# Kernel tuning notes

Measured on AMD Instinct MI355X. Metric: run time of the kernel, lower is better.

The kernel has to match this reference:

```python
import jax, jax.numpy as jnp
import numpy as np
import math

D = 512
LAMBDA_DRIFT = 0.3

def _sinusoid(pos, d):
    # pos: [B, T] float positions (1..T); returns [B, T, d]
    half = d // 2
    div = jnp.exp(-math.log(10000.0) * (2.0 * jnp.arange(half, dtype=jnp.float32) / d))
    ang = pos[..., None] * div  # [B,T,half]
    pe = jnp.stack([jnp.sin(ang), jnp.cos(ang)], axis=-1)  # [B,T,half,2]
    return pe.reshape(pos.shape + (d,))

def _lin(x, W, b):
    return x @ W + b

def setup_inputs() -> dict:
    key = jax.random.key(0)
    ks = jax.random.split(key, 30)
    B, T, L = 4, 16, 1024
    def w(k, fan_in, fan_out):
        return jax.random.normal(k, (fan_in, fan_out), dtype=jnp.float32) / np.sqrt(fan_in)
    inp = {
        'x': jax.random.normal(ks[0], (B, L, D), dtype=jnp.float32),
        'memory_snapshot': jax.random.normal(ks[1], (B, T, L, D), dtype=jnp.float32),
        'delta_W': w(ks[2], D, D), 'delta_b': jnp.zeros((D,), jnp.float32),
        'xproj_W': w(ks[3], D, D), 'xproj_b': jnp.zeros((D,), jnp.float32),
        'phys_W': w(ks[4], D, D), 'phys_b': jnp.zeros((D,), jnp.float32),
        'gate_W': w(ks[5], 3 * D, D), 'gate_b': jnp.zeros((D,), jnp.float32),
        'outp_W': w(ks[6], D, D), 'outp_b': jnp.zeros((D,), jnp.float32),
        'seq_W': w(ks[7], D, D), 'seq_b': jnp.zeros((D,), jnp.float32),
        'q_W': w(ks[8], D, D), 'q_b': jnp.zeros((D,), jnp.float32),
        'mem_W': w(ks[9], D, D), 'mem_b': jnp.zeros((D,), jnp.float32),
        'curd_W': w(ks[10], D, D), 'curd_b': jnp.zeros((D,), jnp.float32),
        'memd_W': w(ks[11], D, D), 'memd_b': jnp.zeros((D,), jnp.float32),
        'fuse_W': w(ks[12], 2 * D, D), 'fuse_b': jnp.zeros((D,), jnp.float32),
    }
    return inp

def reference(x, memory_snapshot,
              delta_W, delta_b, xproj_W, xproj_b, phys_W, phys_b,
              gate_W, gate_b, outp_W, outp_b, seq_W, seq_b,
              q_W, q_b, mem_W, mem_b, curd_W, curd_b,
              memd_W, memd_b, fuse_W, fuse_b):
    B, T, L, Dm = memory_snapshot.shape
    # physical trajectory = last memory slot
    x_phys = memory_snapshot[:, -1]                      # [B,L,D]
    # --- DriftCorrectionExtractor ---
    delta = x - x_phys
    delta_feat = _lin(delta, delta_W, delta_b)
    x_feat = _lin(x, xproj_W, xproj_b)
    phys_feat = _lin(x_phys, phys_W, phys_b)
    g = jax.nn.sigmoid(_lin(jnp.concatenate([delta, x, x_phys], -1), gate_W, gate_b))
    raw_memory = _lin(g * delta_feat + (1.0 - g) * (x_feat - phys_feat), outp_W, outp_b)
    # --- sequential positional embedding on memory time axis ---
    pos = jnp.broadcast_to(jnp.arange(1, T + 1, dtype=jnp.float32)[None, :], (B, T))
    pos_emb = _lin(_sinusoid(pos, Dm), seq_W, seq_b)     # [B,T,D]
    memory = memory_snapshot + pos_emb[:, :, None, :]    # [B,T,L,D]
    # --- content score ---
    q_global = _lin((x + raw_memory).mean(axis=1), q_W, q_b)        # [B,D]
    memory_global = _lin(memory.mean(axis=2), mem_W, mem_b)          # [B,T,D]
    content_score = jnp.einsum('bd,btd->bt', q_global, memory_global) / math.sqrt(Dm)
    # --- drift score ---
    cur_drift = _lin(delta.mean(axis=1), curd_W, curd_b)             # [B,D]
    mem_delta = jnp.concatenate(
        [memory[:, :1], memory[:, 1:] - memory[:, :-1]], axis=1)     # [B,T,L,D]
    mem_drift = _lin(mem_delta.mean(axis=2), memd_W, memd_b)         # [B,T,D]
    drift_score = -jnp.mean((cur_drift[:, None, :] - mem_drift) ** 2, axis=-1)
    time_attn = jax.nn.softmax(content_score + LAMBDA_DRIFT * drift_score, axis=1)
    enhanced = jnp.einsum('bt,btld->bld', time_attn, memory)
    fuse_g = jax.nn.sigmoid(_lin(jnp.concatenate([x, enhanced], -1), fuse_W, fuse_b))
    return x + raw_memory + fuse_g * enhanced
```

## Files before the change

### kernel.cpp

```cpp
#include <hip/hip_runtime.h>
#include <hip/hip_bf16.h>
#include <math.h>

typedef __attribute__((ext_vector_type(8))) short short8;
typedef __attribute__((ext_vector_type(4))) float floatx4;

__device__ __forceinline__ short f2bits(float f) {
    union { float f; unsigned u; } cv; cv.f = f;
    unsigned u = cv.u;
    u += 0x7fffu + ((u >> 16) & 1u);
    return (short)(u >> 16);
}

__device__ __forceinline__ floatx4 mfma16(short8 a, short8 b, floatx4 c) {
    return __builtin_amdgcn_mfma_f32_16x16x32_bf16(a, b, c, 0, 0, 0);
}

typedef const __attribute__((address_space(1))) unsigned int* gas_ptr;
typedef __attribute__((address_space(3))) unsigned int* las_ptr;

__device__ __forceinline__ void gl2lds16(const short* g, short* l) {
    __builtin_amdgcn_global_load_lds((gas_ptr)g, (las_ptr)l, 16, 0, 0);
}

__global__ __launch_bounds__(256) void k_tr2(
    const float* __restrict__ w_delta, const float* __restrict__ w_xproj,
    const float* __restrict__ w_phys,  const float* __restrict__ w_outp,
    const float* __restrict__ w_gate,  const float* __restrict__ w_fuse,
    short* __restrict__ bt_delta, short* __restrict__ bt_xproj,
    short* __restrict__ bt_phys,  short* __restrict__ bt_outp,
    short* __restrict__ bt_gate,  short* __restrict__ bt_fuse)
{
    __shared__ float sf[32 * 33];
    int id = blockIdx.x;
    const float* W; short* BT; int K; int local;
    if (id < 256)        { W = w_delta; BT = bt_delta; K = 512;  local = id; }
    else if (id < 512)   { W = w_xproj; BT = bt_xproj; K = 512;  local = id - 256; }
    else if (id < 768)   { W = w_phys;  BT = bt_phys;  K = 512;  local = id - 512; }
    else if (id < 1024)  { W = w_outp;  BT = bt_outp;  K = 512;  local = id - 768; }
    else if (id < 1792)  { W = w_gate;  BT = bt_gate;  K = 1536; local = id - 1024; }
    else                 { W = w_fuse;  BT = bt_fuse;  K = 1024; local = id - 1792; }
    int kt = local >> 4, nt = local & 15;
    int t = threadIdx.x;
    int r = t >> 3, c = (t & 7) * 4;
    float4 v = *(const float4*)(W + (size_t)(kt * 32 + r) * 512 + nt * 32 + c);
    sf[r * 33 + c + 0] = v.x; sf[r * 33 + c + 1] = v.y;
    sf[r * 33 + c + 2] = v.z; sf[r * 33 + c + 3] = v.w;
    __syncthreads();
    int n = t >> 3, k4 = (t & 7) * 4;
    short4 o;
    o.x = f2bits(sf[(k4 + 0) * 33 + n]);
    o.y = f2bits(sf[(k4 + 1) * 33 + n]);
    o.z = f2bits(sf[(k4 + 2) * 33 + n]);
    o.w = f2bits(sf[(k4 + 3) * 33 + n]);
    *(short4*)(BT + (size_t)(nt * 32 + n) * K + kt * 32 + k4) = o;
}

__global__ __launch_bounds__(256) void k_prep(const float* __restrict__ x,
                                              const float* __restrict__ ms,
                                              short* __restrict__ A1)
{
    int gid = blockIdx.x * 256 + threadIdx.x;
    int r = gid >> 7;
    int c4 = (gid & 127) << 2;
    int b = r >> 10, l = r & 1023;
    float4 xv = *(const float4*)(x + (size_t)r * 512 + c4);
    float4 pv = *(const float4*)(ms + ((size_t)(b * 16 + 15) * 1024 + l) * 512 + c4);
    short4 xb, pb, db;
    xb.x = f2bits(xv.x); xb.y = f2bits(xv.y); xb.z = f2bits(xv.z); xb.w = f2bits(xv.w);
    pb.x = f2bits(pv.x); pb.y = f2bits(pv.y); pb.z = f2bits(pv.z); pb.w = f2bits(pv.w);
    db.x = f2bits(xv.x - pv.x); db.y = f2bits(xv.y - pv.y);
    db.z = f2bits(xv.z - pv.z); db.w = f2bits(xv.w - pv.w);
    short* row = A1 + (size_t)r * 1536;
    *(short4*)(row + c4) = db;
    *(short4*)(row + 512 + c4) = xb;
    *(short4*)(row + 1024 + c4) = pb;
}

__global__ __launch_bounds__(128) void k_msum(const float* __restrict__ ms, float* __restrict__ msum)
{
    int bt = blockIdx.x >> 3;
    int chunk = blockIdx.x & 7;
    int c4 = threadIdx.x << 2;
    const float* base = ms + ((size_t)bt * 1024 + chunk * 128) * 512 + c4;
    float a0 = 0, a1 = 0, a2 = 0, a3 = 0;
    for (int l = 0; l < 128; ++l) {
        float4 v = *(const float4*)(base + (size_t)l * 512);
        a0 += v.x; a1 += v.y; a2 += v.z; a3 += v.w;
    }
    float* dst = msum + bt * 512 + c4;
    atomicAdd(dst + 0, a0); atomicAdd(dst + 1, a1);
    atomicAdd(dst + 2, a2); atomicAdd(dst + 3, a3);
}

__global__ __launch_bounds__(128) void k_dmean(const float* __restrict__ x, const float* __restrict__ ms,
                                               float* __restrict__ dmean)
{
    int b = blockIdx.x >> 3, chunk = blockIdx.x & 7;
    int c4 = threadIdx.x << 2;
    float a0 = 0, a1 = 0, a2 = 0, a3 = 0;
    for (int l = 0; l < 128; ++l) {
        int r = b * 1024 + chunk * 128 + l;
        int lr = chunk * 128 + l;
        float4 xv = *(const float4*)(x + (size_t)r * 512 + c4);
        float4 pv = *(const float4*)(ms + ((size_t)(b * 16 + 15) * 1024 + lr) * 512 + c4);
        a0 += xv.x - pv.x; a1 += xv.y - pv.y; a2 += xv.z - pv.z; a3 += xv.w - pv.w;
    }
    float* dst = dmean + b * 512 + c4;
    atomicAdd(dst + 0, a0); atomicAdd(dst + 1, a1);
    atomicAdd(dst + 2, a2); atomicAdd(dst + 3, a3);
}

__global__ __launch_bounds__(128) void k_rmean(const float* __restrict__ x, const float* __restrict__ rawm,
                                               float* __restrict__ xrm)
{
    int b = blockIdx.x >> 3, chunk = blockIdx.x & 7;
    int c4 = threadIdx.x << 2;
    float a0 = 0, a1 = 0, a2 = 0, a3 = 0;
    for (int l = 0; l < 128; ++l) {
        size_t idx = ((size_t)(b * 1024 + chunk * 128 + l)) * 512 + c4;
        float4 v = *(const float4*)(x + idx);
        float4 rm = *(const float4*)(rawm + idx);
        a0 += v.x + rm.x; a1 += v.y + rm.y; a2 += v.z + rm.z; a3 += v.w + rm.w;
    }
    float* dst = xrm + b * 512 + c4;
    atomicAdd(dst + 0, a0); atomicAdd(dst + 1, a1);
    atomicAdd(dst + 2, a2); atomicAdd(dst + 3, a3);
}

__global__ __launch_bounds__(256) void gemm_h_t(
    const short* __restrict__ A1,
    const short* __restrict__ BTd, const short* __restrict__ BTx,
    const short* __restrict__ BTp, const short* __restrict__ BTg,
    const float* __restrict__ bd, const float* __restrict__ bx,
    const float* __restrict__ bp, const float* __restrict__ bg,
    short* __restrict__ H)
{
    __shared__ __align__(16) short As[2048], Bgs[2048], Bss[2048];
    int bm = blockIdx.x >> 3, bn = blockIdx.x & 7;
    int t = threadIdx.x;
    int lane = t & 63;
    int wm = (t >> 6) & 1, wn = t >> 7;
    int l15 = lane & 15, quad = lane >> 4;

    int srow = t >> 2;
    int sc = ((t & 3) - (srow >> 1)) & 3;
    const short* ga  = A1  + (size_t)(bm * 64 + srow) * 1536 + sc * 8;
    const short* ggb = BTg + (size_t)(bn * 64 + srow) * 1536 + sc * 8;
    const short* gsd = BTd + (size_t)(bn * 64 + srow) * 512 + sc * 8;
    const short* gsx = BTx + (size_t)(bn * 64 + srow) * 512 + sc * 8;
    const short* gsp = BTp + (size_t)(bn * 64 + srow) * 512 + sc * 8;
    short* la  = As  + t * 8;
    short* lgb = Bgs + t * 8;
    short* lsb = Bss + t * 8;

    int arow = wm * 32 + l15;
    int brow = wn * 32 + l15;
    const short* ra0 = As  + arow * 32 + ((quad + (arow >> 1)) & 3) * 8;
    const short* ra1 = ra0 + 512;
    const short* rg0 = Bgs + brow * 32 + ((quad + (brow >> 1)) & 3) * 8;
    const short* rg1 = rg0 + 512;
    const short* rs0 = Bss + brow * 32 + ((quad + (brow >> 1)) & 3) * 8;
    const short* rs1 = rs0 + 512;

    floatx4 g00 = {0,0,0,0}, g01 = {0,0,0,0}, g10 = {0,0,0,0}, g11 = {0,0,0,0};
    floatx4 d00 = {0,0,0,0}, d01 = {0,0,0,0}, d10 = {0,0,0,0}, d11 = {0,0,0,0};
    floatx4 x00 = {0,0,0,0}, x01 = {0,0,0,0}, x10 = {0,0,0,0}, x11 = {0,0,0,0};
    floatx4 p00 = {0,0,0,0}, p01 = {0,0,0,0}, p10 = {0,0,0,0}, p11 = {0,0,0,0};

#define HPHASE(GSB, S00, S01, S10, S11, KBASE)                                  \
    for (int k0 = 0; k0 < 512; k0 += 32) {                                      \
        gl2lds16(ga + KBASE + k0, la);                                          \
        gl2lds16(ggb + KBASE + k0, lgb);                                        \
        gl2lds16(GSB + k0, lsb);                                                \
        __syncthreads();                                                        \
        short8 a0 = *(const short8*)ra0; short8 a1 = *(const short8*)ra1;       \
        short8 c0 = *(const short8*)rg0; short8 c1 = *(const short8*)rg1;       \
        short8 e0 = *(const short8*)rs0; short8 e1 = *(const short8*)rs1;       \
        g00 = mfma16(a0, c0, g00); g01 = mfma16(a0, c1, g01);                   \
        g10 = mfma16(a1, c0, g10); g11 = mfma16(a1, c1, g11);                   \
        S00 = mfma16(a0, e0, S00); S01 = mfma16(a0, e1, S01);                   \
        S10 = mfma16(a1, e0, S10); S11 = mfma16(a1, e1, S11);                   \
        __syncthreads();                                                        \
    }

    HPHASE(gsd, d00, d01, d10, d11, 0)
    HPHASE(gsx, x00, x01, x10, x11, 512)
    HPHASE(gsp, p00, p01, p10, p11, 1024)
#undef HPHASE

    floatx4 G[2][2] = {{g00, g01}, {g10, g11}};
    floatx4 Dd[2][2] = {{d00, d01}, {d10, d11}};
    floatx4 Xx[2][2] = {{x00, x01}, {x10, x11}};
    floatx4 Pp[2][2] = {{p00, p01}, {p10, p11}};
    int colb = bn * 64 + wn * 32 + l15;
    int rowb = bm * 64 + wm * 32 + quad * 4;
    for (int ni = 0; ni < 2; ++ni) {
        int col = colb + ni * 16;
        float vbd = bd[col], vbx = bx[col], vbp = bp[col], vbg = bg[col];
        for (int mi = 0; mi < 2; ++mi) {
            for (int r = 0; r < 4; ++r) {
                int row = rowb + mi * 16 + r;
                float gv = 1.f / (1.f + expf(-(G[mi][ni][r] + vbg)));
                float h = gv * (Dd[mi][ni][r] + vbd)
                        + (1.f - gv) * ((Xx[mi][ni][r] + vbx) - (Pp[mi][ni][r] + vbp));
                H[(size_t)row * 512 + col] = f2bits(h);
            }
        }
    }
}

template<int MODE>
__global__ __launch_bounds__(256) void gemm_t(
    const short* __restrict__ A, int lda,
    const short* __restrict__ BT, int K,
    const float* __restrict__ bias, float* __restrict__ C,
    const float* __restrict__ xsrc, const float* __restrict__ rawm,
    const float* __restrict__ enh, float* __restrict__ outp)
{
    __shared__ __align__(16) short As[2048], Bs[2048];
    int bm = blockIdx.x >> 3, bn = blockIdx.x & 7;
    int t = threadIdx.x;
    int lane = t & 63;
    int wm = (t >> 6) & 1, wn = t >> 7;
    int l15 = lane & 15, quad = lane >> 4;

    int srow = t >> 2;
    int sc = ((t & 3) - (srow >> 1)) & 3;
    const short* ga = A + (size_t)(bm * 64 + srow) * lda + sc * 8;
    const short* gb = BT + (size_t)(bn * 64 + srow) * K + sc * 8;
    short* la = As + t * 8;
    short* lb = Bs + t * 8;

    int arow = wm * 32 + l15;
    int brow = wn * 32 + l15;
    const short* ra0 = As + arow * 32 + ((quad + (arow >> 1)) & 3) * 8;
    const short* ra1 = ra0 + 512;
    const short* rb0 = Bs + brow * 32 + ((quad + (brow >> 1)) & 3) * 8;
    const short* rb1 = rb0 + 512;

    floatx4 a00 = {0,0,0,0}, a01 = {0,0,0,0}, a10 = {0,0,0,0}, a11 = {0,0,0,0};

    for (int k0 = 0; k0 < K; k0 += 32) {
        gl2lds16(ga + k0, la);
        gl2lds16(gb + k0, lb);
        __syncthreads();
        short8 a0 = *(const short8*)ra0; short8 a1 = *(const short8*)ra1;
        short8 b0 = *(const short8*)rb0; short8 b1 = *(const short8*)rb1;
        a00 = mfma16(a0, b0, a00); a01 = mfma16(a0, b1, a01);
        a10 = mfma16(a1, b0, a10); a11 = mfma16(a1, b1, a11);
        __syncthreads();
    }

    floatx4 Acc[2][2] = {{a00, a01}, {a10, a11}};
    int colb = bn * 64 + wn * 32 + l15;
    int rowb = bm * 64 + wm * 32 + quad * 4;
    for (int ni = 0; ni < 2; ++ni) {
        int col = colb + ni * 16;
        float bv = bias[col];
        for (int mi = 0; mi < 2; ++mi) {
            for (int r = 0; r < 4; ++r) {
                int row = rowb + mi * 16 + r;
                size_t idx = (size_t)row * 512 + col;
                float v = Acc[mi][ni][r] + bv;
                if (MODE == 0) {
                    C[idx] = v;
                } else {
                    float fg = 1.f / (1.f + expf(-v));
                    outp[idx] = xsrc[idx] + rawm[idx] + fg * enh[idx];
                }
            }
        }
    }
}

__global__ __launch_bounds__(256) void k_pe(const float* __restrict__ seqW, const float* __restrict__ seqb,
                                            float* __restrict__ pe_proj)
{
    __shared__ float pe[512];
    int t = blockIdx.x;
    for (int d = threadIdx.x; d < 512; d += 256) {
        int i = d >> 1;
        float div = expf(-9.210340371976184f * (2.f * i / 512.f));
        float ang = (float)(t + 1) * div;
        pe[d] = (d & 1) ? cosf(ang) : sinf(ang);
    }
    __syncthreads();
    for (int n = threadIdx.x; n < 512; n += 256) {
        float acc = 0.f;
        for (int d = 0; d < 512; ++d) acc += pe[d] * seqW[(size_t)d * 512 + n];
        pe_proj[t * 512 + n] = acc + seqb[n];
    }
}

__global__ __launch_bounds__(128) void k_sbuild(const float* __restrict__ msum,
                                                const float* __restrict__ pe_proj,
                                                const float* __restrict__ xrm,
                                                const float* __restrict__ dmean,
                                                float* __restrict__ SM)
{
    int row = blockIdx.x;
    int c4 = threadIdx.x << 2;
    const float invL = 1.f / 1024.f;
    float4 o;
    if (row < 64) {
        int tt = row & 15;
        float4 m = *(const float4*)(msum + row * 512 + c4);
        float4 p = *(const float4*)(pe_proj + tt * 512 + c4);
        o.x = m.x * invL + p.x; o.y = m.y * invL + p.y;
        o.z = m.z * invL + p.z; o.w = m.w * invL + p.w;
    } else if (row < 128) {
        int j = row - 64, tt = j & 15;
        float4 m = *(const float4*)(msum + j * 512 + c4);
        float4 p = *(const float4*)(pe_proj + tt * 512 + c4);
        o.x = m.x * invL + p.x; o.y = m.y * invL + p.y;
        o.z = m.z * invL + p.z; o.w = m.w * invL + p.w;
        if (tt > 0) {
            float4 m2 = *(const float4*)(msum + (j - 1) * 512 + c4);
            float4 p2 = *(const float4*)(pe_proj + (tt - 1) * 512 + c4);
            o.x -= m2.x * invL + p2.x; o.y -= m2.y * invL + p2.y;
            o.z -= m2.z * invL + p2.z; o.w -= m2.w * invL + p2.w;
        }
    } else if (row < 132) {
        float4 m = *(const float4*)(xrm + (row - 128) * 512 + c4);
        o.x = m.x * invL; o.y = m.y * invL; o.z = m.z * invL; o.w = m.w * invL;
    } else {
        float4 m = *(const float4*)(dmean + (row - 132) * 512 + c4);
        o.x = m.x * invL; o.y = m.y * invL; o.z = m.z * invL; o.w = m.w * invL;
    }
    *(float4*)(SM + row * 512 + c4) = o;
}

__global__ __launch_bounds__(256) void k_mid2(const float* __restrict__ SM,
                                              const float* __restrict__ memW,  const float* __restrict__ memb,
                                              const float* __restrict__ memdW, const float* __restrict__ memdb,
                                              const float* __restrict__ qW,    const float* __restrict__ qb,
                                              const float* __restrict__ curdW, const float* __restrict__ curdb,
                                              float* __restrict__ mg, float* __restrict__ mdrift,
                                              float* __restrict__ qg, float* __restrict__ curd)
{
    __shared__ float sS[4 * 512];
    __shared__ float part[128 * 16];
    int blk = blockIdx.x;
    const float* W; const float* bias; const float* S; float* out;
    if (blk < 16)      { W = memW;  bias = memb;  S = SM + blk * 4 * 512;          out = mg + blk * 4 * 512; }
    else if (blk < 32) { W = memdW; bias = memdb; S = SM + (64 + (blk - 16) * 4) * 512; out = mdrift + (blk - 16) * 4 * 512; }
    else if (blk == 32){ W = qW;    bias = qb;    S = SM + 128 * 512;              out = qg; }
    else               { W = curdW; bias = curdb; S = SM + 132 * 512;              out = curd; }
    int t = threadIdx.x;
    for (int i = t * 4; i < 2048; i += 1024) *(float4*)(sS + i) = *(const float4*)(S + i);
    __syncthreads();
    int tn = t & 127, dph = t >> 7;
    int n4 = tn * 4;
    float4 acc0 = {0,0,0,0}, acc1 = {0,0,0,0}, acc2 = {0,0,0,0}, acc3 = {0,0,0,0};
    const float* wp = W + (size_t)(dph * 256) * 512 + n4;
    const float* sp = sS + dph * 256;
#pragma unroll 4
    for (int d = 0; d < 256; ++d) {
        float4 w = *(const float4*)(wp + (size_t)d * 512);
        float s0 = sp[d], s1 = sp[512 + d], s2 = sp[1024 + d], s3 = sp[1536 + d];
        acc0.x += s0 * w.x; acc0.y += s0 * w.y; acc0.z += s0 * w.z; acc0.w += s0 * w.w;
        acc1.x += s1 * w.x; acc1.y += s1 * w.y; acc1.z += s1 * w.z; acc1.w += s1 * w.w;
        acc2.x += s2 * w.x; acc2.y += s2 * w.y; acc2.z += s2 * w.z; acc2.w += s2 * w.w;
        acc3.x += s3 * w.x; acc3.y += s3 * w.y; acc3.z += s3 * w.z; acc3.w += s3 * w.w;
    }
    if (dph == 1) {
        *(float4*)(part + tn * 16 + 0)  = acc0;
        *(float4*)(part + tn * 16 + 4)  = acc1;
        *(float4*)(part + tn * 16 + 8)  = acc2;
        *(float4*)(part + tn * 16 + 12) = acc3;
    }
    __syncthreads();
    if (dph == 0) {
        float4 bv = *(const float4*)(bias + n4);
        float4 p0 = *(const float4*)(part + tn * 16 + 0);
        float4 p1 = *(const float4*)(part + tn * 16 + 4);
        float4 p2 = *(const float4*)(part + tn * 16 + 8);
        float4 p3 = *(const float4*)(part + tn * 16 + 12);
        float4 o0, o1, o2, o3;
        o0.x = acc0.x + p0.x + bv.x; o0.y = acc0.y + p0.y + bv.y; o0.z = acc0.z + p0.z + bv.z; o0.w = acc0.w + p0.w + bv.w;
        o1.x = acc1.x + p1.x + bv.x; o1.y = acc1.y + p1.y + bv.y; o1.z = acc1.z + p1.z + bv.z; o1.w = acc1.w + p1.w + bv.w;
        o2.x = acc2.x + p2.x + bv.x; o2.y = acc2.y + p2.y + bv.y; o2.z = acc2.z + p2.z + bv.z; o2.w = acc2.w + p2.w + bv.w;
        o3.x = acc3.x + p3.x + bv.x; o3.y = acc3.y + p3.y + bv.y; o3.z = acc3.z + p3.z + bv.z; o3.w = acc3.w + p3.w + bv.w;
        *(float4*)(out + 0 * 512 + n4) = o0;
        *(float4*)(out + 1 * 512 + n4) = o1;
        *(float4*)(out + 2 * 512 + n4) = o2;
        *(float4*)(out + 3 * 512 + n4) = o3;
    }
}

__global__ __launch_bounds__(256) void k_attn(const float* __restrict__ qg, const float* __restrict__ mg,
                                              const float* __restrict__ curd, const float* __restrict__ mdrift,
                                              const float* __restrict__ pe_proj,
                                              float* __restrict__ attn, float* __restrict__ pe_att)
{
    int b = blockIdx.x;
    __shared__ float sq[512], sc[512], sscore[16], sattn[16];
    for (int d = threadIdx.x; d < 512; d += 256) { sq[d] = qg[b * 512 + d]; sc[d] = curd[b * 512 + d]; }
    __syncthreads();
    int wv = threadIdx.x >> 6, lane = threadIdx.x & 63;
    for (int t = wv; t < 16; t += 4) {
        float cs = 0.f, dsum = 0.f;
        const float* mgp = mg + (size_t)(b * 16 + t) * 512;
        const float* mdp = mdrift + (size_t)(b * 16 + t) * 512;
        for (int d = lane; d < 512; d += 64) {
            cs += sq[d] * mgp[d];
            float df_ = sc[d] - mdp[d];
            dsum += df_ * df_;
        }
        for (int off = 32; off; off >>= 1) { cs += __shfl_down(cs, off); dsum += __shfl_down(dsum, off); }
        if (lane == 0) sscore[t] = cs * (1.f / 22.627416997969522f) + 0.3f * (-dsum / 512.f);
    }
    __syncthreads();
    if (threadIdx.x == 0) {
        float mx = -1e30f;
        for (int t = 0; t < 16; ++t) mx = fmaxf(mx, sscore[t]);
        float s = 0.f;
        for (int t = 0; t < 16; ++t) { float e = expf(sscore[t] - mx); sattn[t] = e; s += e; }
        for (int t = 0; t < 16; ++t) { sattn[t] /= s; attn[b * 16 + t] = sattn[t]; }
    }
    __syncthreads();
    for (int n = threadIdx.x; n < 512; n += 256) {
        float a = 0.f;
        for (int t = 0; t < 16; ++t) a += sattn[t] * pe_proj[t * 512 + n];
        pe_att[b * 512 + n] = a;
    }
}

__global__ __launch_bounds__(128) void k_enh(const float* __restrict__ ms, const float* __restrict__ x,
                                             const float* __restrict__ attn, const float* __restrict__ pe_att,
                                             float* __restrict__ enh, short* __restrict__ A2)
{
    int r = blockIdx.x;
    int b = r >> 10, l = r & 1023;
    __shared__ float sa[16];
    if (threadIdx.x < 16) sa[threadIdx.x] = attn[b * 16 + threadIdx.x];
    __syncthreads();
    int c4 = threadIdx.x << 2;
    float4 pa = *(const float4*)(pe_att + b * 512 + c4);
    float a0 = pa.x, a1 = pa.y, a2 = pa.z, a3 = pa.w;
    const float* base = ms + ((size_t)(b * 16) * 1024 + l) * 512 + c4;
    for (int t = 0; t < 16; ++t) {
        float4 v = *(const float4*)(base + (size_t)t * 1024 * 512);
        float w = sa[t];
        a0 += w * v.x; a1 += w * v.y; a2 += w * v.z; a3 += w * v.w;
    }
    size_t oi = (size_t)r * 512 + c4;
    float4 ef; ef.x = a0; ef.y = a1; ef.z = a2; ef.w = a3;
    *(float4*)(enh + oi) = ef;
    float4 xv = *(const float4*)(x + oi);
    short4 xb, eb;
    xb.x = f2bits(xv.x); xb.y = f2bits(xv.y); xb.z = f2bits(xv.z); xb.w = f2bits(xv.w);
    eb.x = f2bits(a0); eb.y = f2bits(a1); eb.z = f2bits(a2); eb.w = f2bits(a3);
    short* arow = A2 + (size_t)r * 1024;
    *(short4*)(arow + c4) = xb;
    *(short4*)(arow + 512 + c4) = eb;
}

extern "C" void kernel_launch(void* const* d_in, const int* in_sizes, int n_in,
                              void* d_out, int out_size, void* d_ws, size_t ws_size,
                              hipStream_t stream)
{
    const float* x       = (const float*)d_in[0];
    const float* ms      = (const float*)d_in[1];
    const float* delta_W = (const float*)d_in[2];  const float* delta_b = (const float*)d_in[3];
    const float* xproj_W = (const float*)d_in[4];  const float* xproj_b = (const float*)d_in[5];
    const float* phys_W  = (const float*)d_in[6];  const float* phys_b  = (const float*)d_in[7];
    const float* gate_W  = (const float*)d_in[8];  const float* gate_b  = (const float*)d_in[9];
    const float* outp_W  = (const float*)d_in[10]; const float* outp_b  = (const float*)d_in[11];
    const float* seq_W   = (const float*)d_in[12]; const float* seq_b   = (const float*)d_in[13];
    const float* q_W     = (const float*)d_in[14]; const float* q_b     = (const float*)d_in[15];
    const float* mem_W   = (const float*)d_in[16]; const float* mem_b   = (const float*)d_in[17];
    const float* curd_W  = (const float*)d_in[18]; const float* curd_b  = (const float*)d_in[19];
    const float* memd_W  = (const float*)d_in[20]; const float* memd_b  = (const float*)d_in[21];
    const float* fuse_W  = (const float*)d_in[22]; const float* fuse_b  = (const float*)d_in[23];
    float* out = (float*)d_out;
    char* wsb = (char*)d_ws;

    short* BT_delta = (short*)(wsb + 0);
    short* BT_xproj = (short*)(wsb + 524288);
    short* BT_phys  = (short*)(wsb + 1048576);
    short* BT_outp  = (short*)(wsb + 1572864);
    short* BT_gate  = (short*)(wsb + 2097152);
    short* BT_fuse  = (short*)(wsb + 3670016);
    short* A1       = (short*)(wsb + 4718592);
    short* H        = (short*)(wsb + 17301504);
    float* RAWM     = (float*)(wsb + 21495808);
    float* ENH      = (float*)(wsb + 29884416);
    short* A2       = (short*)(wsb + 38273024);
    float* MSUM     = (float*)(wsb + 46661632);
    float* DMEAN    = (float*)(wsb + 46792704);
    float* XRM      = (float*)(wsb + 46800896);
    float* PEPROJ   = (float*)(wsb + 46809088);
    float* MG       = (float*)(wsb + 46841856);
    float* MDRIFT   = (float*)(wsb + 46972928);
    float* QG       = (float*)(wsb + 47104000);
    float* CURD     = (float*)(wsb + 47112192);
    float* ATTN     = (float*)(wsb + 47120384);
    float* PEATT    = (float*)(wsb + 47121408);
    float* SM       = (float*)(wsb + 47129600);

    hipMemsetAsync(wsb + 46661632, 0, 131072 + 8192 + 8192, stream);

    k_tr2<<<2304, 256, 0, stream>>>(delta_W, xproj_W, phys_W, outp_W, gate_W, fuse_W,
                                    BT_delta, BT_xproj, BT_phys, BT_outp, BT_gate, BT_fuse);
    k_pe<<<16, 256, 0, stream>>>(seq_W, seq_b, PEPROJ);
    k_prep<<<2048, 256, 0, stream>>>(x, ms, A1);
    k_msum<<<512, 128, 0, stream>>>(ms, MSUM);
    k_dmean<<<32, 128, 0, stream>>>(x, ms, DMEAN);

    gemm_h_t<<<512, 256, 0, stream>>>(A1, BT_delta, BT_xproj, BT_phys, BT_gate,
                                      delta_b, xproj_b, phys_b, gate_b, H);
    gemm_t<0><<<512, 256, 0, stream>>>(H, 512, BT_outp, 512, outp_b, RAWM,
                                       nullptr, nullptr, nullptr, nullptr);
    k_rmean<<<32, 128, 0, stream>>>(x, RAWM, XRM);

    k_sbuild<<<136, 128, 0, stream>>>(MSUM, PEPROJ, XRM, DMEAN, SM);
    k_mid2<<<34, 256, 0, stream>>>(SM, mem_W, mem_b, memd_W, memd_b,
                                   q_W, q_b, curd_W, curd_b,
                                   MG, MDRIFT, QG, CURD);
    k_attn<<<4, 256, 0, stream>>>(QG, MG, CURD, MDRIFT, PEPROJ, ATTN, PEATT);
    k_enh<<<4096, 128, 0, stream>>>(ms, x, ATTN, PEATT, ENH, A2);

    gemm_t<2><<<512, 256, 0, stream>>>(A2, 1024, BT_fuse, 1024, fuse_b, nullptr,
                                       x, RAWM, ENH, out);
}
```

Before: 448.5 us.

## Merge front-end kernels, fold S-build into mid kernel, deepen GEMM K tiles

Five front-end launches (weight transpose, positional projection, bf16 prep, memory sum, delta mean) become one multi-role kernel, and the reduction blocks now use 256 threads. The S-matrix build kernel is folded into k_mid2's shared-memory load. gemm_h_t moves to K=64 tiles with more MFMAs per barrier, and gemm_t uses a larger M tile (128 rows), which halves its grid to 256 blocks. The aim is fewer launches and barriers; the risk is lower occupancy from larger LDS and fewer blocks on the GEMMs, plus the k_pe branch serialising inside the combined grid.

```diff
diff --git a/kernel.cpp b/kernel.cpp
--- a/kernel.cpp
+++ b/kernel.cpp
@@ -23,92 +23,103 @@
     __builtin_amdgcn_global_load_lds((gas_ptr)g, (las_ptr)l, 16, 0, 0);
 }
 
-__global__ __launch_bounds__(256) void k_tr2(
+__global__ __launch_bounds__(256) void k_front(
     const float* __restrict__ w_delta, const float* __restrict__ w_xproj,
     const float* __restrict__ w_phys,  const float* __restrict__ w_outp,
     const float* __restrict__ w_gate,  const float* __restrict__ w_fuse,
     short* __restrict__ bt_delta, short* __restrict__ bt_xproj,
     short* __restrict__ bt_phys,  short* __restrict__ bt_outp,
-    short* __restrict__ bt_gate,  short* __restrict__ bt_fuse)
+    short* __restrict__ bt_gate,  short* __restrict__ bt_fuse,
+    const float* __restrict__ x, const float* __restrict__ ms,
+    const float* __restrict__ seqW, const float* __restrict__ seqb,
+    short* __restrict__ A1, float* __restrict__ pe_proj,
+    float* __restrict__ msum, float* __restrict__ dmean)
 {
     __shared__ float sf[32 * 33];
-    int id = blockIdx.x;
-    const float* W; short* BT; int K; int local;
-    if (id < 256)        { W = w_delta; BT = bt_delta; K = 512;  local = id; }
-    else if (id < 512)   { W = w_xproj; BT = bt_xproj; K = 512;  local = id - 256; }
-    else if (id < 768)   { W = w_phys;  BT = bt_phys;  K = 512;  local = id - 512; }
-    else if (id < 1024)  { W = w_outp;  BT = bt_outp;  K = 512;  local = id - 768; }
-    else if (id < 1792)  { W = w_gate;  BT = bt_gate;  K = 1536; local = id - 1024; }
-    else                 { W = w_fuse;  BT = bt_fuse;  K = 1024; local = id - 1792; }
-    int kt = local >> 4, nt = local & 15;
+    __shared__ float pe[512];
+    int bi = blockIdx.x;
     int t = threadIdx.x;
-    int r = t >> 3, c = (t & 7) * 4;
-    float4 v = *(const float4*)(W + (size_t)(kt * 32 + r) * 512 + nt * 32 + c);
-    sf[r * 33 + c + 0] = v.x; sf[r * 33 + c + 1] = v.y;
-    sf[r * 33 + c + 2] = v.z; sf[r * 33 + c + 3] = v.w;
-    __syncthreads();
-    int n = t >> 3, k4 = (t & 7) * 4;
-    short4 o;
-    o.x = f2bits(sf[(k4 + 0) * 33 + n]);
-    o.y = f2bits(sf[(k4 + 1) * 33 + n]);
-    o.z = f2bits(sf[(k4 + 2) * 33 + n]);
-    o.w = f2bits(sf[(k4 + 3) * 33 + n]);
-    *(short4*)(BT + (size_t)(nt * 32 + n) * K + kt * 32 + k4) = o;
-}
-
-__global__ __launch_bounds__(256) void k_prep(const float* __restrict__ x,
-                                              const float* __restrict__ ms,
-                                              short* __restrict__ A1)
-{
-    int gid = blockIdx.x * 256 + threadIdx.x;
-    int r = gid >> 7;
-    int c4 = (gid & 127) << 2;
-    int b = r >> 10, l = r & 1023;
-    float4 xv = *(const float4*)(x + (size_t)r * 512 + c4);
-    float4 pv = *(const float4*)(ms + ((size_t)(b * 16 + 15) * 1024 + l) * 512 + c4);
-    short4 xb, pb, db;
-    xb.x = f2bits(xv.x); xb.y = f2bits(xv.y); xb.z = f2bits(xv.z); xb.w = f2bits(xv.w);
-    pb.x = f2bits(pv.x); pb.y = f2bits(pv.y); pb.z = f2bits(pv.z); pb.w = f2bits(pv.w);
-    db.x = f2bits(xv.x - pv.x); db.y = f2bits(xv.y - pv.y);
-    db.z = f2bits(xv.z - pv.z); db.w = f2bits(xv.w - pv.w);
-    short* row = A1 + (size_t)r * 1536;
-    *(short4*)(row + c4) = db;
-    *(short4*)(row + 512 + c4) = xb;
-    *(short4*)(row + 1024 + c4) = pb;
-}
-
-__global__ __launch_bounds__(128) void k_msum(const float* __restrict__ ms, float* __restrict__ msum)
-{
-    int bt = blockIdx.x >> 3;
-    int chunk = blockIdx.x & 7;
-    int c4 = threadIdx.x << 2;
-    const float* base = ms + ((size_t)bt * 1024 + chunk * 128) * 512 + c4;
-    float a0 = 0, a1 = 0, a2 = 0, a3 = 0;
-    for (int l = 0; l < 128; ++l) {
-        float4 v = *(const float4*)(base + (size_t)l * 512);
-        a0 += v.x; a1 += v.y; a2 += v.z; a3 += v.w;
-    }
-    float* dst = msum + bt * 512 + c4;
-    atomicAdd(dst + 0, a0); atomicAdd(dst + 1, a1);
-    atomicAdd(dst + 2, a2); atomicAdd(dst + 3, a3);
-}
-
-__global__ __launch_bounds__(128) void k_dmean(const float* __restrict__ x, const float* __restrict__ ms,
-                                               float* __restrict__ dmean)
-{
-    int b = blockIdx.x >> 3, chunk = blockIdx.x & 7;
-    int c4 = threadIdx.x << 2;
-    float a0 = 0, a1 = 0, a2 = 0, a3 = 0;
-    for (int l = 0; l < 128; ++l) {
-        int r = b * 1024 + chunk * 128 + l;
-        int lr = chunk * 128 + l;
+    if (bi < 2304) {
+        int id = bi;
+        const float* W; short* BT; int K; int local;
+        if (id < 256)        { W = w_delta; BT = bt_delta; K = 512;  local = id; }
+        else if (id < 512)   { W = w_xproj; BT = bt_xproj; K = 512;  local = id - 256; }
+        else if (id < 768)   { W = w_phys;  BT = bt_phys;  K = 512;  local = id - 512; }
+        else if (id < 1024)  { W = w_outp;  BT = bt_outp;  K = 512;  local = id - 768; }
+        else if (id < 1792)  { W = w_gate;  BT = bt_gate;  K = 1536; local = id - 1024; }
+        else                 { W = w_fuse;  BT = bt_fuse;  K = 1024; local = id - 1792; }
+        int kt = local >> 4, nt = local & 15;
+        int r = t >> 3, c = (t & 7) * 4;
+        float4 v = *(const float4*)(W + (size_t)(kt * 32 + r) * 512 + nt * 32 + c);
+        sf[r * 33 + c + 0] = v.x; sf[r * 33 + c + 1] = v.y;
+        sf[r * 33 + c + 2] = v.z; sf[r * 33 + c + 3] = v.w;
+        __syncthreads();
+        int n = t >> 3, k4 = (t & 7) * 4;
+        short4 o;
+        o.x = f2bits(sf[(k4 + 0) * 33 + n]);
+        o.y = f2bits(sf[(k4 + 1) * 33 + n]);
+        o.z = f2bits(sf[(k4 + 2) * 33 + n]);
+        o.w = f2bits(sf[(k4 + 3) * 33 + n]);
+        *(short4*)(BT + (size_t)(nt * 32 + n) * K + kt * 32 + k4) = o;
+    } else if (bi < 2320) {
+        int tt = bi - 2304;
+        for (int d = t; d < 512; d += 256) {
+            int i = d >> 1;
+            float div = expf(-9.210340371976184f * (2.f * i / 512.f));
+            float ang = (float)(tt + 1) * div;
+            pe[d] = (d & 1) ? cosf(ang) : sinf(ang);
+        }
+        __syncthreads();
+        for (int n = t; n < 512; n += 256) {
+            float acc = 0.f;
+            for (int d = 0; d < 512; ++d) acc += pe[d] * seqW[(size_t)d * 512 + n];
+            pe_proj[tt * 512 + n] = acc + seqb[n];
+        }
+    } else if (bi < 4368) {
+        int gid = (bi - 2320) * 256 + t;
+        int r = gid >> 7;
+        int c4 = (gid & 127) << 2;
+        int b = r >> 10, l = r & 1023;
         float4 xv = *(const float4*)(x + (size_t)r * 512 + c4);
-        float4 pv = *(const float4*)(ms + ((size_t)(b * 16 + 15) * 1024 + lr) * 512 + c4);
-        a0 += xv.x - pv.x; a1 += xv.y - pv.y; a2 += xv.z - pv.z; a3 += xv.w - pv.w;
-    }
-    float* dst = dmean + b * 512 + c4;
-    atomicAdd(dst + 0, a0); atomicAdd(dst + 1, a1);
-    atomicAdd(dst + 2, a2); atomicAdd(dst + 3, a3);
+        float4 pv = *(const float4*)(ms + ((size_t)(b * 16 + 15) * 1024 + l) * 512 + c4);
+        short4 xb, pb, db;
+        xb.x = f2bits(xv.x); xb.y = f2bits(xv.y); xb.z = f2bits(xv.z); xb.w = f2bits(xv.w);
+        pb.x = f2bits(pv.x); pb.y = f2bits(pv.y); pb.z = f2bits(pv.z); pb.w = f2bits(pv.w);
+        db.x = f2bits(xv.x - pv.x); db.y = f2bits(xv.y - pv.y);
+        db.z = f2bits(xv.z - pv.z); db.w = f2bits(xv.w - pv.w);
+        short* row = A1 + (size_t)r * 1536;
+        *(short4*)(row + c4) = db;
+        *(short4*)(row + 512 + c4) = xb;
+        *(short4*)(row + 1024 + c4) = pb;
+    } else if (bi < 4880) {
+        int blk = bi - 4368;
+        int bt = blk >> 3, chunk = blk & 7;
+        int half = t >> 7, c4 = (t & 127) << 2;
+        const float* base = ms + ((size_t)(bt * 1024 + chunk * 128 + half * 64)) * 512 + c4;
+        float a0 = 0, a1 = 0, a2 = 0, a3 = 0;
+        for (int l = 0; l < 64; ++l) {
+            float4 v = *(const float4*)(base + (size_t)l * 512);
+            a0 += v.x; a1 += v.y; a2 += v.z; a3 += v.w;
+        }
+        float* dst = msum + bt * 512 + c4;
+        atomicAdd(dst + 0, a0); atomicAdd(dst + 1, a1);
+        atomicAdd(dst + 2, a2); atomicAdd(dst + 3, a3);
+    } else {
+        int blk = bi - 4880;
+        int b = blk >> 3, chunk = blk & 7;
+        int half = t >> 7, c4 = (t & 127) << 2;
+        float a0 = 0, a1 = 0, a2 = 0, a3 = 0;
+        for (int l = 0; l < 64; ++l) {
+            int lr = chunk * 128 + half * 64 + l;
+            int r = b * 1024 + lr;
+            float4 xv = *(const float4*)(x + (size_t)r * 512 + c4);
+            float4 pv = *(const float4*)(ms + ((size_t)(b * 16 + 15) * 1024 + lr) * 512 + c4);
+            a0 += xv.x - pv.x; a1 += xv.y - pv.y; a2 += xv.z - pv.z; a3 += xv.w - pv.w;
+        }
+        float* dst = dmean + b * 512 + c4;
+        atomicAdd(dst + 0, a0); atomicAdd(dst + 1, a1);
+        atomicAdd(dst + 2, a2); atomicAdd(dst + 3, a3);
+    }
 }
 
 __global__ __launch_bounds__(128) void k_rmean(const float* __restrict__ x, const float* __restrict__ rawm,
@@ -136,77 +147,95 @@
     const float* __restrict__ bp, const float* __restrict__ bg,
     short* __restrict__ H)
 {
-    __shared__ __align__(16) short As[2048], Bgs[2048], Bss[2048];
+    __shared__ __align__(16) short As[4096], Bgs[4096], Bss[4096];
     int bm = blockIdx.x >> 3, bn = blockIdx.x & 7;
-    int t = threadIdx.x;
-    int lane = t & 63;
+    int t = threadIdx.x, lane = t & 63;
     int wm = (t >> 6) & 1, wn = t >> 7;
     int l15 = lane & 15, quad = lane >> 4;
-
-    int srow = t >> 2;
-    int sc = ((t & 3) - (srow >> 1)) & 3;
-    const short* ga  = A1  + (size_t)(bm * 64 + srow) * 1536 + sc * 8;
-    const short* ggb = BTg + (size_t)(bn * 64 + srow) * 1536 + sc * 8;
-    const short* gsd = BTd + (size_t)(bn * 64 + srow) * 512 + sc * 8;
-    const short* gsx = BTx + (size_t)(bn * 64 + srow) * 512 + sc * 8;
-    const short* gsp = BTp + (size_t)(bn * 64 + srow) * 512 + sc * 8;
-    short* la  = As  + t * 8;
-    short* lgb = Bgs + t * 8;
-    short* lsb = Bss + t * 8;
-
-    int arow = wm * 32 + l15;
-    int brow = wn * 32 + l15;
-    const short* ra0 = As  + arow * 32 + ((quad + (arow >> 1)) & 3) * 8;
-    const short* ra1 = ra0 + 512;
-    const short* rg0 = Bgs + brow * 32 + ((quad + (brow >> 1)) & 3) * 8;
-    const short* rg1 = rg0 + 512;
-    const short* rs0 = Bss + brow * 32 + ((quad + (brow >> 1)) & 3) * 8;
-    const short* rs1 = rs0 + 512;
-
-    floatx4 g00 = {0,0,0,0}, g01 = {0,0,0,0}, g10 = {0,0,0,0}, g11 = {0,0,0,0};
-    floatx4 d00 = {0,0,0,0}, d01 = {0,0,0,0}, d10 = {0,0,0,0}, d11 = {0,0,0,0};
-    floatx4 x00 = {0,0,0,0}, x01 = {0,0,0,0}, x10 = {0,0,0,0}, x11 = {0,0,0,0};
-    floatx4 p00 = {0,0,0,0}, p01 = {0,0,0,0}, p10 = {0,0,0,0}, p11 = {0,0,0,0};
-
-#define HPHASE(GSB, S00, S01, S10, S11, KBASE)                                  \
-    for (int k0 = 0; k0 < 512; k0 += 32) {                                      \
-        gl2lds16(ga + KBASE + k0, la);                                          \
-        gl2lds16(ggb + KBASE + k0, lgb);                                        \
-        gl2lds16(GSB + k0, lsb);                                                \
-        __syncthreads();                                                        \
-        short8 a0 = *(const short8*)ra0; short8 a1 = *(const short8*)ra1;       \
-        short8 c0 = *(const short8*)rg0; short8 c1 = *(const short8*)rg1;       \
-        short8 e0 = *(const short8*)rs0; short8 e1 = *(const short8*)rs1;       \
-        g00 = mfma16(a0, c0, g00); g01 = mfma16(a0, c1, g01);                   \
-        g10 = mfma16(a1, c0, g10); g11 = mfma16(a1, c1, g11);                   \
-        S00 = mfma16(a0, e0, S00); S01 = mfma16(a0, e1, S01);                   \
-        S10 = mfma16(a1, e0, S10); S11 = mfma16(a1, e1, S11);                   \
-        __syncthreads();                                                        \
-    }
-
-    HPHASE(gsd, d00, d01, d10, d11, 0)
-    HPHASE(gsx, x00, x01, x10, x11, 512)
-    HPHASE(gsp, p00, p01, p10, p11, 1024)
+    int tr8 = t >> 3, pc = t & 7;
+
+    int row0 = tr8, row1 = 32 + tr8;
+    int lc0 = (pc - (row0 >> 1)) & 7, lc1 = (pc - (row1 >> 1)) & 7;
+    const short* gaA0 = A1 + (size_t)(bm * 64 + row0) * 1536 + lc0 * 8;
+    const short* gaA1 = A1 + (size_t)(bm * 64 + row1) * 1536 + lc1 * 8;
+    const short* gaG0 = BTg + (size_t)(bn * 64 + row0) * 1536 + lc0 * 8;
+    const short* gaG1 = BTg + (size_t)(bn * 64 + row1) * 1536 + lc1 * 8;
+    const short* gd0 = BTd + (size_t)(bn * 64 + row0) * 512 + lc0 * 8;
+    const short* gd1 = BTd + (size_t)(bn * 64 + row1) * 512 + lc1 * 8;
+    const short* gx0 = BTx + (size_t)(bn * 64 + row0) * 512 + lc0 * 8;
+    const short* gx1 = BTx + (size_t)(bn * 64 + row1) * 512 + lc1 * 8;
+    const short* gp0 = BTp + (size_t)(bn * 64 + row0) * 512 + lc0 * 8;
+    const short* gp1 = BTp + (size_t)(bn * 64 + row1) * 512 + lc1 * 8;
+    short* ldA0 = As + t * 8;  short* ldA1 = As + 2048 + t * 8;
+    short* ldG0 = Bgs + t * 8; short* ldG1 = Bgs + 2048 + t * 8;
+    short* ldS0 = Bss + t * 8; short* ldS1 = Bss + 2048 + t * 8;
+
+    const short *ra[2][2], *rg[2][2], *rs[2][2];
+#pragma unroll
+    for (int mi = 0; mi < 2; ++mi)
+#pragma unroll
+        for (int ki = 0; ki < 2; ++ki) {
+            int row = wm * 32 + mi * 16 + l15;
+            int off = row * 64 + ((ki * 4 + quad + (row >> 1)) & 7) * 8;
+            ra[mi][ki] = As + off;
+            int rowb = wn * 32 + mi * 16 + l15;
+            int offb = rowb * 64 + ((ki * 4 + quad + (rowb >> 1)) & 7) * 8;
+            rg[mi][ki] = Bgs + offb;
+            rs[mi][ki] = Bss + offb;
+        }
+
+    floatx4 accg[2][2], accd[2][2], accx[2][2], accp[2][2];
+#pragma unroll
+    for (int i = 0; i < 2; ++i)
+#pragma unroll
+        for (int j = 0; j < 2; ++j) {
+            accg[i][j] = (floatx4){0,0,0,0}; accd[i][j] = (floatx4){0,0,0,0};
+            accx[i][j] = (floatx4){0,0,0,0}; accp[i][j] = (floatx4){0,0,0,0};
+        }
+
+#define HPHASE(S0, S1, ACC, KB)                                                  \
+    for (int k0 = 0; k0 < 512; k0 += 64) {                                       \
+        gl2lds16(gaA0 + KB + k0, ldA0); gl2lds16(gaA1 + KB + k0, ldA1);          \
+        gl2lds16(gaG0 + KB + k0, ldG0); gl2lds16(gaG1 + KB + k0, ldG1);          \
+        gl2lds16(S0 + k0, ldS0);        gl2lds16(S1 + k0, ldS1);                 \
+        __syncthreads();                                                         \
+        short8 av[2][2], gv[2][2], sv[2][2];                                     \
+        _Pragma("unroll") for (int mi = 0; mi < 2; ++mi)                         \
+        _Pragma("unroll") for (int ki = 0; ki < 2; ++ki) {                       \
+            av[mi][ki] = *(const short8*)ra[mi][ki];                             \
+            gv[mi][ki] = *(const short8*)rg[mi][ki];                             \
+            sv[mi][ki] = *(const short8*)rs[mi][ki];                             \
+        }                                                                        \
+        _Pragma("unroll") for (int ki = 0; ki < 2; ++ki)                         \
+        _Pragma("unroll") for (int mi = 0; mi < 2; ++mi)                         \
+        _Pragma("unroll") for (int ni = 0; ni < 2; ++ni) {                       \
+            accg[mi][ni] = mfma16(av[mi][ki], gv[ni][ki], accg[mi][ni]);         \
+            ACC[mi][ni]  = mfma16(av[mi][ki], sv[ni][ki], ACC[mi][ni]);          \
+        }                                                                        \
+        __syncthreads();                                                         \
+    }
+
+    HPHASE(gd0, gd1, accd, 0)
+    HPHASE(gx0, gx1, accx, 512)
+    HPHASE(gp0, gp1, accp, 1024)
 #undef HPHASE
 
-    floatx4 G[2][2] = {{g00, g01}, {g10, g11}};
-    floatx4 Dd[2][2] = {{d00, d01}, {d10, d11}};
-    floatx4 Xx[2][2] = {{x00, x01}, {x10, x11}};
-    floatx4 Pp[2][2] = {{p00, p01}, {p10, p11}};
     int colb = bn * 64 + wn * 32 + l15;
     int rowb = bm * 64 + wm * 32 + quad * 4;
+#pragma unroll
     for (int ni = 0; ni < 2; ++ni) {
         int col = colb + ni * 16;
         float vbd = bd[col], vbx = bx[col], vbp = bp[col], vbg = bg[col];
-        for (int mi = 0; mi < 2; ++mi) {
+#pragma unroll
+        for (int mi = 0; mi < 2; ++mi)
+#pragma unroll
             for (int r = 0; r < 4; ++r) {
                 int row = rowb + mi * 16 + r;
-                float gv = 1.f / (1.f + expf(-(G[mi][ni][r] + vbg)));
-                float h = gv * (Dd[mi][ni][r] + vbd)
-                        + (1.f - gv) * ((Xx[mi][ni][r] + vbx) - (Pp[mi][ni][r] + vbp));
+                float gv = 1.f / (1.f + expf(-(accg[mi][ni][r] + vbg)));
+                float h = gv * (accd[mi][ni][r] + vbd)
+                        + (1.f - gv) * ((accx[mi][ni][r] + vbx) - (accp[mi][ni][r] + vbp));
                 H[(size_t)row * 512 + col] = f2bits(h);
             }
-        }
     }
 }
 
@@ -218,51 +247,90 @@
     const float* __restrict__ xsrc, const float* __restrict__ rawm,
     const float* __restrict__ enh, float* __restrict__ outp)
 {
-    __shared__ __align__(16) short As[2048], Bs[2048];
+    __shared__ __align__(16) short As[8192], Bs[4096];
     int bm = blockIdx.x >> 3, bn = blockIdx.x & 7;
-    int t = threadIdx.x;
-    int lane = t & 63;
+    int t = threadIdx.x, lane = t & 63;
     int wm = (t >> 6) & 1, wn = t >> 7;
     int l15 = lane & 15, quad = lane >> 4;
-
-    int srow = t >> 2;
-    int sc = ((t & 3) - (srow >> 1)) & 3;
-    const short* ga = A + (size_t)(bm * 64 + srow) * lda + sc * 8;
-    const short* gb = BT + (size_t)(bn * 64 + srow) * K + sc * 8;
-    short* la = As + t * 8;
-    short* lb = Bs + t * 8;
-
-    int arow = wm * 32 + l15;
-    int brow = wn * 32 + l15;
-    const short* ra0 = As + arow * 32 + ((quad + (arow >> 1)) & 3) * 8;
-    const short* ra1 = ra0 + 512;
-    const short* rb0 = Bs + brow * 32 + ((quad + (brow >> 1)) & 3) * 8;
-    const short* rb1 = rb0 + 512;
-
-    floatx4 a00 = {0,0,0,0}, a01 = {0,0,0,0}, a10 = {0,0,0,0}, a11 = {0,0,0,0};
-
-    for (int k0 = 0; k0 < K; k0 += 32) {
-        gl2lds16(ga + k0, la);
-        gl2lds16(gb + k0, lb);
+    int tr8 = t >> 3, pc = t & 7;
+
+    const short* gaA[4]; short* ldA[4];
+    const short* gaB[2]; short* ldB[2];
+#pragma unroll
+    for (int s = 0; s < 4; ++s) {
+        int row = s * 32 + tr8;
+        int lc = (pc - (row >> 1)) & 7;
+        gaA[s] = A + (size_t)(bm * 128 + row) * lda + lc * 8;
+        ldA[s] = As + s * 2048 + t * 8;
+    }
+#pragma unroll
+    for (int s = 0; s < 2; ++s) {
+        int row = s * 32 + tr8;
+        int lc = (pc - (row >> 1)) & 7;
+        gaB[s] = BT + (size_t)(bn * 64 + row) * K + lc * 8;
+        ldB[s] = Bs + s * 2048 + t * 8;
+    }
+
+    const short *ra[4][2], *rb[2][2];
+#pragma unroll
+    for (int mi = 0; mi < 4; ++mi)
+#pragma unroll
+        for (int ki = 0; ki < 2; ++ki) {
+            int row = wm * 64 + mi * 16 + l15;
+            ra[mi][ki] = As + row * 64 + ((ki * 4 + quad + (row >> 1)) & 7) * 8;
+        }
+#pragma unroll
+    for (int ni = 0; ni < 2; ++ni)
+#pragma unroll
+        for (int ki = 0; ki < 2; ++ki) {
+            int row = wn * 32 + ni * 16 + l15;
+            rb[ni][ki] = Bs + row * 64 + ((ki * 4 + quad + (row >> 1)) & 7) * 8;
+        }
+
+    floatx4 acc[4][2];
+#pragma unroll
+    for (int mi = 0; mi < 4; ++mi)
+#pragma unroll
+        for (int ni = 0; ni < 2; ++ni) acc[mi][ni] = (floatx4){0,0,0,0};
+
+    for (int k0 = 0; k0 < K; k0 += 64) {
+#pragma unroll
+        for (int s = 0; s < 4; ++s) gl2lds16(gaA[s] + k0, ldA[s]);
+#pragma unroll
+        for (int s = 0; s < 2; ++s) gl2lds16(gaB[s] + k0, ldB[s]);
         __syncthreads();
-        short8 a0 = *(const short8*)ra0; short8 a1 = *(const short8*)ra1;
-        short8 b0 = *(const short8*)rb0; short8 b1 = *(const short8*)rb1;
-        a00 = mfma16(a0, b0, a00); a01 = mfma16(a0, b1, a01);
-        a10 = mfma16(a1, b0, a10); a11 = mfma16(a1, b1, a11);
+        short8 av[4][2], bv[2][2];
+#pragma unroll
+        for (int mi = 0; mi < 4; ++mi)
+#pragma unroll
+            for (int ki = 0; ki < 2; ++ki) av[mi][ki] = *(const short8*)ra[mi][ki];
+#pragma unroll
+        for (int ni = 0; ni < 2; ++ni)
+#pragma unroll
+            for (int ki = 0; ki < 2; ++ki) bv[ni][ki] = *(const short8*)rb[ni][ki];
+#pragma unroll
+        for (int ki = 0; ki < 2; ++ki)
+#pragma unroll
+            for (int mi = 0; mi < 4; ++mi)
+#pragma unroll
+                for (int ni = 0; ni < 2; ++ni)
+                    acc[mi][ni] = mfma16(av[mi][ki], bv[ni][ki], acc[mi][ni]);
         __syncthreads();
     }
 
-    floatx4 Acc[2][2] = {{a00, a01}, {a10, a11}};
     int colb = bn * 64 + wn * 32 + l15;
-    int rowb = bm * 64 + wm * 32 + quad * 4;
+    int rowb = bm * 128 + wm * 64 + quad * 4;
+#pragma unroll
     for (int ni = 0; ni < 2; ++ni) {
         int col = colb + ni * 16;
-        float bv = bias[col];
-        for (int mi = 0; mi < 2; ++mi) {
+        float bv2 = bias[col];
+#pragma unroll
+        for (int mi = 0; mi < 4; ++mi)
+#pragma unroll
             for (int r = 0; r < 4; ++r) {
                 int row = rowb + mi * 16 + r;
                 size_t idx = (size_t)row * 512 + col;
-                float v = Acc[mi][ni][r] + bv;
+                float v = acc[mi][ni][r] + bv2;
                 if (MODE == 0) {
                     C[idx] = v;
                 } else {
@@ -270,68 +338,13 @@
                     outp[idx] = xsrc[idx] + rawm[idx] + fg * enh[idx];
                 }
             }
-        }
-    }
-}
-
-__global__ __launch_bounds__(256) void k_pe(const float* __restrict__ seqW, const float* __restrict__ seqb,
-                                            float* __restrict__ pe_proj)
-{
-    __shared__ float pe[512];
-    int t = blockIdx.x;
-    for (int d = threadIdx.x; d < 512; d += 256) {
-        int i = d >> 1;
-        float div = expf(-9.210340371976184f * (2.f * i / 512.f));
-        float ang = (float)(t + 1) * div;
-        pe[d] = (d & 1) ? cosf(ang) : sinf(ang);
-    }
-    __syncthreads();
-    for (int n = threadIdx.x; n < 512; n += 256) {
-        float acc = 0.f;
-        for (int d = 0; d < 512; ++d) acc += pe[d] * seqW[(size_t)d * 512 + n];
-        pe_proj[t * 512 + n] = acc + seqb[n];
-    }
-}
-
-__global__ __launch_bounds__(128) void k_sbuild(const float* __restrict__ msum,
-                                                const float* __restrict__ pe_proj,
-                                                const float* __restrict__ xrm,
-                                                const float* __restrict__ dmean,
-                                                float* __restrict__ SM)
-{
-    int row = blockIdx.x;
-    int c4 = threadIdx.x << 2;
-    const float invL = 1.f / 1024.f;
-    float4 o;
-    if (row < 64) {
-        int tt = row & 15;
-        float4 m = *(const float4*)(msum + row * 512 + c4);
-        float4 p = *(const float4*)(pe_proj + tt * 512 + c4);
-        o.x = m.x * invL + p.x; o.y = m.y * invL + p.y;
-        o.z = m.z * invL + p.z; o.w = m.w * invL + p.w;
-    } else if (row < 128) {
-        int j = row - 64, tt = j & 15;
-        float4 m = *(const float4*)(msum + j * 512 + c4);
-        float4 p = *(const float4*)(pe_proj + tt * 512 + c4);
-        o.x = m.x * invL + p.x; o.y = m.y * invL + p.y;
-        o.z = m.z * invL + p.z; o.w = m.w * invL + p.w;
-        if (tt > 0) {
-            float4 m2 = *(const float4*)(msum + (j - 1) * 512 + c4);
-            float4 p2 = *(const float4*)(pe_proj + (tt - 1) * 512 + c4);
-            o.x -= m2.x * invL + p2.x; o.y -= m2.y * invL + p2.y;
-            o.z -= m2.z * invL + p2.z; o.w -= m2.w * invL + p2.w;
-        }
-    } else if (row < 132) {
-        float4 m = *(const float4*)(xrm + (row - 128) * 512 + c4);
-        o.x = m.x * invL; o.y = m.y * invL; o.z = m.z * invL; o.w = m.w * invL;
-    } else {
-        float4 m = *(const float4*)(dmean + (row - 132) * 512 + c4);
-        o.x = m.x * invL; o.y = m.y * invL; o.z = m.z * invL; o.w = m.w * invL;
-    }
-    *(float4*)(SM + row * 512 + c4) = o;
-}
-
-__global__ __launch_bounds__(256) void k_mid2(const float* __restrict__ SM,
+    }
+}
+
+__global__ __launch_bounds__(256) void k_mid2(const float* __restrict__ msum,
+                                              const float* __restrict__ pe_proj,
+                                              const float* __restrict__ xrm,
+                                              const float* __restrict__ dmean,
                                               const float* __restrict__ memW,  const float* __restrict__ memb,
                                               const float* __restrict__ memdW, const float* __restrict__ memdb,
                                               const float* __restrict__ qW,    const float* __restrict__ qb,
@@ -342,13 +355,43 @@
     __shared__ float sS[4 * 512];
     __shared__ float part[128 * 16];
     int blk = blockIdx.x;
-    const float* W; const float* bias; const float* S; float* out;
-    if (blk < 16)      { W = memW;  bias = memb;  S = SM + blk * 4 * 512;          out = mg + blk * 4 * 512; }
-    else if (blk < 32) { W = memdW; bias = memdb; S = SM + (64 + (blk - 16) * 4) * 512; out = mdrift + (blk - 16) * 4 * 512; }
-    else if (blk == 32){ W = qW;    bias = qb;    S = SM + 128 * 512;              out = qg; }
-    else               { W = curdW; bias = curdb; S = SM + 132 * 512;              out = curd; }
+    const float invL = 1.f / 1024.f;
+    const float* W; const float* bias; float* out;
+    if (blk < 16)      { W = memW;  bias = memb;  out = mg + blk * 2048; }
+    else if (blk < 32) { W = memdW; bias = memdb; out = mdrift + (blk - 16) * 2048; }
+    else if (blk == 32){ W = qW;    bias = qb;    out = qg; }
+    else               { W = curdW; bias = curdb; out = curd; }
     int t = threadIdx.x;
-    for (int i = t * 4; i < 2048; i += 1024) *(float4*)(sS + i) = *(const float4*)(S + i);
+    for (int e = t * 4; e < 2048; e += 1024) {
+        int r = e >> 9, d = e & 511;
+        float4 o;
+        if (blk < 16) {
+            int gr = blk * 4 + r; int tt = gr & 15;
+            float4 m = *(const float4*)(msum + gr * 512 + d);
+            float4 p = *(const float4*)(pe_proj + tt * 512 + d);
+            o.x = m.x * invL + p.x; o.y = m.y * invL + p.y;
+            o.z = m.z * invL + p.z; o.w = m.w * invL + p.w;
+        } else if (blk < 32) {
+            int j = (blk - 16) * 4 + r; int tt = j & 15;
+            float4 m = *(const float4*)(msum + j * 512 + d);
+            float4 p = *(const float4*)(pe_proj + tt * 512 + d);
+            o.x = m.x * invL + p.x; o.y = m.y * invL + p.y;
+            o.z = m.z * invL + p.z; o.w = m.w * invL + p.w;
+            if (tt > 0) {
+                float4 m2 = *(const float4*)(msum + (j - 1) * 512 + d);
+                float4 p2 = *(const float4*)(pe_proj + (tt - 1) * 512 + d);
+                o.x -= m2.x * invL + p2.x; o.y -= m2.y * invL + p2.y;
+                o.z -= m2.z * invL + p2.z; o.w -= m2.w * invL + p2.w;
+            }
+        } else if (blk == 32) {
+            float4 m = *(const float4*)(xrm + e);
+            o.x = m.x * invL; o.y = m.y * invL; o.z = m.z * invL; o.w = m.w * invL;
+        } else {
+            float4 m = *(const float4*)(dmean + e);
+            o.x = m.x * invL; o.y = m.y * invL; o.z = m.z * invL; o.w = m.w * invL;
+        }
+        *(float4*)(sS + e) = o;
+    }
     __syncthreads();
     int tn = t & 127, dph = t >> 7;
     int n4 = tn * 4;
@@ -498,30 +541,26 @@
     float* CURD     = (float*)(wsb + 47112192);
     float* ATTN     = (float*)(wsb + 47120384);
     float* PEATT    = (float*)(wsb + 47121408);
-    float* SM       = (float*)(wsb + 47129600);
 
     hipMemsetAsync(wsb + 46661632, 0, 131072 + 8192 + 8192, stream);
 
-    k_tr2<<<2304, 256, 0, stream>>>(delta_W, xproj_W, phys_W, outp_W, gate_W, fuse_W,
-                                    BT_delta, BT_xproj, BT_phys, BT_outp, BT_gate, BT_fuse);
-    k_pe<<<16, 256, 0, stream>>>(seq_W, seq_b, PEPROJ);
-    k_prep<<<2048, 256, 0, stream>>>(x, ms, A1);
-    k_msum<<<512, 128, 0, stream>>>(ms, MSUM);
-    k_dmean<<<32, 128, 0, stream>>>(x, ms, DMEAN);
+    k_front<<<4912, 256, 0, stream>>>(delta_W, xproj_W, phys_W, outp_W, gate_W, fuse_W,
+                                      BT_delta, BT_xproj, BT_phys, BT_outp, BT_gate, BT_fuse,
+                                      x, ms, seq_W, seq_b, A1, PEPROJ, MSUM, DMEAN);
 
     gemm_h_t<<<512, 256, 0, stream>>>(A1, BT_delta, BT_xproj, BT_phys, BT_gate,
                                       delta_b, xproj_b, phys_b, gate_b, H);
-    gemm_t<0><<<512, 256, 0, stream>>>(H, 512, BT_outp, 512, outp_b, RAWM,
+    gemm_t<0><<<256, 256, 0, stream>>>(H, 512, BT_outp, 512, outp_b, RAWM,
                                        nullptr, nullptr, nullptr, nullptr);
     k_rmean<<<32, 128, 0, stream>>>(x, RAWM, XRM);
 
-    k_sbuild<<<136, 128, 0, stream>>>(MSUM, PEPROJ, XRM, DMEAN, SM);
-    k_mid2<<<34, 256, 0, stream>>>(SM, mem_W, mem_b, memd_W, memd_b,
+    k_mid2<<<34, 256, 0, stream>>>(MSUM, PEPROJ, XRM, DMEAN,
+                                   mem_W, mem_b, memd_W, memd_b,
                                    q_W, q_b, curd_W, curd_b,
                                    MG, MDRIFT, QG, CURD);
     k_attn<<<4, 256, 0, stream>>>(QG, MG, CURD, MDRIFT, PEPROJ, ATTN, PEATT);
     k_enh<<<4096, 128, 0, stream>>>(ms, x, ATTN, PEATT, ENH, A2);
 
-    gemm_t<2><<<512, 256, 0, stream>>>(A2, 1024, BT_fuse, 1024, fuse_b, nullptr,
+    gemm_t<2><<<256, 256, 0, stream>>>(A2, 1024, BT_fuse, 1024, fuse_b, nullptr,
                                        x, RAWM, ENH, out);
 }
```

Result: faster. 410.7 us (-8.4%).
